# Optimization experiments

Hardware: AMD Instinct MI355X
Metric: run time of the kernel (lower is better)

The kernel has to match this reference:

```python
import jax, jax.numpy as jnp
import numpy as np

# Model hyperparameters (match init_kwargs / module defaults)
B, P, F_IN, H, K, OUT = 1024, 256, 8, 16, 8, 1


def _lin_init(key, out_f, in_f, bias=True):
    # torch nn.Linear default: U(-1/sqrt(in), 1/sqrt(in))
    kw, kb = jax.random.split(key)
    bound = 1.0 / np.sqrt(in_f)
    W = jax.random.uniform(kw, (out_f, in_f), jnp.float32, -bound, bound)
    if bias:
        b = jax.random.uniform(kb, (out_f,), jnp.float32, -bound, bound)
        return W, b
    return W


def setup_inputs() -> dict:
    key = jax.random.key(0)
    ks = jax.random.split(key, 7)
    x = jax.random.normal(ks[0], (B, P * F_IN), jnp.float32)
    W1 = _lin_init(ks[1], H, F_IN, bias=False)          # part_encode[0], bias=False
    W2, b2 = _lin_init(ks[2], H, H)                      # part_encode[2]
    W3, b3 = _lin_init(ks[3], H, H)                      # part_encode[4]
    We, be = _lin_init(ks[4], H, 2 * H)                  # edge MLP Linear(2H, H)
    Wo1, bo1 = _lin_init(ks[5], H // 2, H)               # output[0]
    Wo2, bo2 = _lin_init(ks[6], OUT, H // 2)             # output[2]
    return {"x": x, "W1": W1, "W2": W2, "b2": b2, "W3": W3, "b3": b3,
            "We": We, "be": be, "Wo1": Wo1, "bo1": bo1, "Wo2": Wo2, "bo2": bo2}


def reference(x, W1, W2, b2, W3, b3, We, be, Wo1, bo1, Wo2, bo2):
    b = x.shape[0]
    # part_encode MLP on flattened particles
    h = x.reshape(b * P, F_IN)
    h = jax.nn.elu(h @ W1.T)
    h = jax.nn.elu(h @ W2.T + b2)
    h = jax.nn.elu(h @ W3.T + b3)
    h = h.reshape(b, P, H)                               # [B,P,H]

    # Dynamic kNN graph per batch element (knn includes self at distance 0,
    # matching torch_cluster.knn on identical query/source sets)
    sq = jnp.sum(h * h, axis=-1)                         # [B,P]
    dist = sq[:, :, None] + sq[:, None, :] - 2.0 * jnp.einsum('bid,bjd->bij', h, h)
    _, idx = jax.lax.top_k(-dist, K)                     # [B,P,K] nearest neighbors

    # Gather neighbor features per graph
    xj = jax.vmap(lambda hb, ib: hb[ib])(h, idx)         # [B,P,K,H]
    xi = jnp.broadcast_to(h[:, :, None, :], xj.shape)    # [B,P,K,H]
    edge = jnp.concatenate([xi, xj - xi], axis=-1)       # [B,P,K,2H]

    # Edge MLP + max aggregation (EdgeConv message nn([x_i, x_j - x_i]), aggr='max')
    m = jax.nn.elu(edge @ We.T + be)                     # [B,P,K,H]
    node = jnp.max(m, axis=2)                            # [B,P,H]

    # avg_pool_x over nodes of each graph
    pooled = jnp.mean(node, axis=1)                      # [B,H]

    # output MLP + sigmoid (act_out=True, batchnorm=False)
    o = jax.nn.elu(pooled @ Wo1.T + bo1)
    o = o @ Wo2.T + bo2
    return jax.nn.sigmoid(o)                             # [B,OUT]
```

## Files before the change

### kernel.cpp

```cpp
#include <hip/hip_runtime.h>
#include <math.h>

#define NB 1024
#define NP 256
#define FIN 8
#define NH 16
#define NK 8

#define REP8A(X)  X(0) X(1) X(2) X(3) X(4) X(5) X(6) X(7)
#define REP16A(X) X(0) X(1) X(2) X(3) X(4) X(5) X(6) X(7) X(8) X(9) X(10) X(11) X(12) X(13) X(14) X(15)
#define REP16B(X) X(0) X(1) X(2) X(3) X(4) X(5) X(6) X(7) X(8) X(9) X(10) X(11) X(12) X(13) X(14) X(15)

typedef short s8v __attribute__((ext_vector_type(8)));
typedef float f4v __attribute__((ext_vector_type(4)));
typedef unsigned int u4v __attribute__((ext_vector_type(4)));

__device__ __forceinline__ float elu_f(float v) {
    return v > 0.f ? v : (__expf(v) - 1.f);
}
__device__ __forceinline__ unsigned bf16r(float f) {
    unsigned u = __float_as_uint(f);
    return (u + 0x7FFFu + ((u >> 16) & 1u)) >> 16;
}
__device__ __forceinline__ float ush2f(unsigned short u) {
    return __uint_as_float(((unsigned)u) << 16);
}

#define CE(a, b) { float lo_ = fminf(a, b), hi_ = fmaxf(a, b); a = lo_; b = hi_; }
#define SORT8(x0,x1,x2,x3,x4,x5,x6,x7) \
    CE(x0,x1) CE(x2,x3) CE(x4,x5) CE(x6,x7) \
    CE(x0,x2) CE(x1,x3) CE(x4,x6) CE(x5,x7) \
    CE(x1,x2) CE(x5,x6) \
    CE(x0,x4) CE(x1,x5) CE(x2,x6) CE(x3,x7) \
    CE(x2,x4) CE(x3,x5) \
    CE(x1,x2) CE(x3,x4) CE(x5,x6)
#define MERGE8P(P,x0,x1,x2,x3,x4,x5,x6,x7) \
    P##0 = fminf(P##0, x7); P##1 = fminf(P##1, x6); P##2 = fminf(P##2, x5); P##3 = fminf(P##3, x4); \
    P##4 = fminf(P##4, x3); P##5 = fminf(P##5, x2); P##6 = fminf(P##6, x1); P##7 = fminf(P##7, x0); \
    CE(P##0,P##4) CE(P##1,P##5) CE(P##2,P##6) CE(P##3,P##7) \
    CE(P##0,P##2) CE(P##1,P##3) CE(P##4,P##6) CE(P##5,P##7) \
    CE(P##0,P##1) CE(P##2,P##3) CE(P##4,P##5) CE(P##6,P##7)

#define KEYV(val, c) __uint_as_float((__float_as_uint((val) + sqp2) & 0xFFFFFF00u) | (unsigned)(c))

__global__ __attribute__((amdgpu_flat_work_group_size(256, 256),
                          amdgpu_waves_per_eu(2, 4)))
void edgenet_kernel(
    const float* __restrict__ gx,
    const float* __restrict__ gW1, const float* __restrict__ gW2, const float* __restrict__ gb2,
    const float* __restrict__ gW3, const float* __restrict__ gb3,
    const float* __restrict__ gWe, const float* __restrict__ gbe,
    const float* __restrict__ gWo1, const float* __restrict__ gbo1,
    const float* __restrict__ gWo2, const float* __restrict__ gbo2,
    float* __restrict__ gout)
{
    const int b  = blockIdx.x;
    const int t  = threadIdx.x;
    const int w  = t >> 6;
    const int lq = (t >> 4) & 3;
    const int lc = t & 15;

    __shared__ __align__(16) unsigned short hF[16][4][136];
    __shared__ __align__(16) float sq2arr[256];
    __shared__ __align__(16) float sbaseA[4][64][17];
    __shared__ __align__(16) uint2 jjarr[4][64];
    __shared__ float spool[64];

    float xi0, xi1, xi2, xi3, xi4, xi5, xi6, xi7;
    {
        const float4* xr = reinterpret_cast<const float4*>(gx + (size_t)b * (NP * FIN) + t * FIN);
        float4 v0 = xr[0], v1 = xr[1];
        xi0 = v0.x; xi1 = v0.y; xi2 = v0.z; xi3 = v0.w;
        xi4 = v1.x; xi5 = v1.y; xi6 = v1.z; xi7 = v1.w;
    }

    float l1_0,l1_1,l1_2,l1_3,l1_4,l1_5,l1_6,l1_7,l1_8,l1_9,l1_10,l1_11,l1_12,l1_13,l1_14,l1_15;
    float l2_0,l2_1,l2_2,l2_3,l2_4,l2_5,l2_6,l2_7,l2_8,l2_9,l2_10,l2_11,l2_12,l2_13,l2_14,l2_15;
    float hp0,hp1,hp2,hp3,hp4,hp5,hp6,hp7,hp8,hp9,hp10,hp11,hp12,hp13,hp14,hp15;

#define L1_BODY(i) s = fmaf(gW1[(o_) * FIN + i], xi##i, s);
#define L1_O(o) { const int o_ = (o); float s = 0.f; REP8A(L1_BODY) l1_##o = elu_f(s); }
    REP16A(L1_O)
#undef L1_O
#undef L1_BODY
#define L2_BODY(i) s = fmaf(gW2[(o_) * NH + i], l1_##i, s);
#define L2_O(o) { const int o_ = (o); float s = gb2[o_]; REP16B(L2_BODY) l2_##o = elu_f(s); }
    REP16A(L2_O)
#undef L2_O
#undef L2_BODY
#define L3_BODY(i) s = fmaf(gW3[(o_) * NH + i], l2_##i, s);
#define L3_O(o) { const int o_ = (o); float s = gb3[o_]; REP16B(L3_BODY) hp##o = elu_f(s); }
    REP16A(L3_O)
#undef L3_O
#undef L3_BODY

    {
        float* sb = &sbaseA[w][t & 63][0];
#define BAS_BODY(i) s = fmaf(gWe[(o_) * 32 + i] - gWe[(o_) * 32 + 16 + i], hp##i, s);
#define BAS_O(o) { const int o_ = (o); float s = gbe[o_]; REP16B(BAS_BODY) sb[o_] = s; }
        REP16A(BAS_O)
#undef BAS_O
#undef BAS_BODY
    }

    s8v eB1;
    {
        float4 wv = *reinterpret_cast<const float4*>(gWe + lc * 32 + 16 + 4 * lq);
        unsigned h0 = bf16r(wv.x), h1 = bf16r(wv.y), h2 = bf16r(wv.z), h3 = bf16r(wv.w);
        unsigned g0 = bf16r(wv.x - ush2f((unsigned short)h0));
        unsigned g1 = bf16r(wv.y - ush2f((unsigned short)h1));
        unsigned g2 = bf16r(wv.z - ush2f((unsigned short)h2));
        unsigned g3 = bf16r(wv.w - ush2f((unsigned short)h3));
        eB1 = (s8v){(short)h0, (short)h1, (short)h2, (short)h3,
                    (short)g0, (short)g1, (short)g2, (short)g3};
    }

    float sqp = 0.f;
#define SQ_I(i) sqp = fmaf(hp##i, hp##i, sqp);
    REP16A(SQ_I)
#undef SQ_I
    const float sqp2 = 0.5f * sqp;

#define PACKQ(q, A, B, C, D) { \
    unsigned ha = bf16r(hp##A), hb = bf16r(hp##B), hc = bf16r(hp##C), hd = bf16r(hp##D); \
    float ra = hp##A - ush2f((unsigned short)ha); \
    float rb = hp##B - ush2f((unsigned short)hb); \
    float rc = hp##C - ush2f((unsigned short)hc); \
    float rd = hp##D - ush2f((unsigned short)hd); \
    unsigned la = bf16r(ra), lb = bf16r(rb), lcc = bf16r(rc), ld = bf16r(rd); \
    u4v pk; pk.x = ha | (hb << 16); pk.y = hc | (hd << 16); \
            pk.z = la | (lb << 16); pk.w = lcc | (ld << 16); \
    *(u4v*)&hF[t >> 4][q][(t & 15) * 8] = pk; }
    PACKQ(0, 0, 1, 2, 3)
    PACKQ(1, 4, 5, 6, 7)
    PACKQ(2, 8, 9, 10, 11)
    PACKQ(3, 12, 13, 14, 15)
#undef PACKQ
    sq2arr[t] = sqp2;
    __syncthreads();

#define LDNAF(i) s8v naf##i; { \
    u4v au = __builtin_bit_cast(u4v, *(const s8v*)&hF[4 * w + (i)][lq][lc * 8]); \
    au.x ^= 0x80008000u; au.y ^= 0x80008000u; au.z ^= 0x80008000u; au.w ^= 0x80008000u; \
    naf##i = __builtin_bit_cast(s8v, au); }
    LDNAF(0) LDNAF(1) LDNAF(2) LDNAF(3)
#undef LDNAF

    float Ra0,Ra1,Ra2,Ra3,Ra4,Ra5,Ra6,Ra7;
    float Rb0,Rb1,Rb2,Rb3,Rb4,Rb5,Rb6,Rb7;
    float Rc0,Rc1,Rc2,Rc3,Rc4,Rc5,Rc6,Rc7;
    float Rd0,Rd1,Rd2,Rd3,Rd4,Rd5,Rd6,Rd7;
    {
        const float big = __uint_as_float(0x7F7FFFFFu);
        Ra0=Ra1=Ra2=Ra3=Ra4=Ra5=Ra6=Ra7 = big;
        Rb0=Rb1=Rb2=Rb3=Rb4=Rb5=Rb6=Rb7 = big;
        Rc0=Rc1=Rc2=Rc3=Rc4=Rc5=Rc6=Rc7 = big;
        Rd0=Rd1=Rd2=Rd3=Rd4=Rd5=Rd6=Rd7 = big;
    }

    for (int jt2 = 0; jt2 < 8; ++jt2) {
        const s8v b1a = *(const s8v*)&hF[2 * jt2][lq][lc * 8];
        const s8v b1b = *(const s8v*)&hF[2 * jt2 + 1][lq][lc * 8];
        const s8v b2a = __builtin_shufflevector(b1a, b1a, 4, 5, 6, 7, 0, 1, 2, 3);
        const s8v b2b = __builtin_shufflevector(b1b, b1b, 4, 5, 6, 7, 0, 1, 2, 3);
        const f4v sqa = *(const f4v*)&sq2arr[32 * jt2 + 4 * lq];
        const f4v sqb = *(const f4v*)&sq2arr[32 * jt2 + 16 + 4 * lq];
        const int c0 = 32 * jt2 + 4 * lq, c1 = c0 + 16;

#define GTT(naf, P) { \
        f4v da = __builtin_amdgcn_mfma_f32_16x16x32_bf16(b1a, naf, sqa, 0, 0, 0); \
        da     = __builtin_amdgcn_mfma_f32_16x16x32_bf16(b2a, naf, da,  0, 0, 0); \
        f4v db = __builtin_amdgcn_mfma_f32_16x16x32_bf16(b1b, naf, sqb, 0, 0, 0); \
        db     = __builtin_amdgcn_mfma_f32_16x16x32_bf16(b2b, naf, db,  0, 0, 0); \
        float k0 = KEYV(da[0], c0 + 0), k1 = KEYV(da[1], c0 + 1); \
        float k2 = KEYV(da[2], c0 + 2), k3 = KEYV(da[3], c0 + 3); \
        float k4 = KEYV(db[0], c1 + 0), k5 = KEYV(db[1], c1 + 1); \
        float k6 = KEYV(db[2], c1 + 2), k7 = KEYV(db[3], c1 + 3); \
        SORT8(k0, k1, k2, k3, k4, k5, k6, k7) \
        MERGE8P(P, k0, k1, k2, k3, k4, k5, k6, k7) }
        GTT(naf0, Ra)
        GTT(naf1, Rb)
        GTT(naf2, Rc)
        GTT(naf3, Rd)
#undef GTT
    }

#define FIN_TT(P, ttc) { \
    { float o0 = __shfl_xor(P##0, 16), o1 = __shfl_xor(P##1, 16), \
            o2 = __shfl_xor(P##2, 16), o3 = __shfl_xor(P##3, 16), \
            o4 = __shfl_xor(P##4, 16), o5 = __shfl_xor(P##5, 16), \
            o6 = __shfl_xor(P##6, 16), o7 = __shfl_xor(P##7, 16); \
      MERGE8P(P, o0, o1, o2, o3, o4, o5, o6, o7) } \
    { float o0 = __shfl_xor(P##0, 32), o1 = __shfl_xor(P##1, 32), \
            o2 = __shfl_xor(P##2, 32), o3 = __shfl_xor(P##3, 32), \
            o4 = __shfl_xor(P##4, 32), o5 = __shfl_xor(P##5, 32), \
            o6 = __shfl_xor(P##6, 32), o7 = __shfl_xor(P##7, 32); \
      MERGE8P(P, o0, o1, o2, o3, o4, o5, o6, o7) } \
    if (lq == (ttc)) { \
        unsigned plo = (__float_as_uint(P##0) & 0xFFu) \
                     | ((__float_as_uint(P##1) & 0xFFu) << 8) \
                     | ((__float_as_uint(P##2) & 0xFFu) << 16) \
                     | ((__float_as_uint(P##3) & 0xFFu) << 24); \
        unsigned phi = (__float_as_uint(P##4) & 0xFFu) \
                     | ((__float_as_uint(P##5) & 0xFFu) << 8) \
                     | ((__float_as_uint(P##6) & 0xFFu) << 16) \
                     | ((__float_as_uint(P##7) & 0xFFu) << 24); \
        jjarr[w][16 * (ttc) + lc] = make_uint2(plo, phi); \
    } }
    FIN_TT(Ra, 0)
    FIN_TT(Rb, 1)
    FIN_TT(Rc, 2)
    FIN_TT(Rd, 3)
#undef FIN_TT

    float psum = 0.f;
    {
        const s8v eB2 = __builtin_shufflevector(eB1, eB1, 4, 5, 6, 7, 0, 1, 2, 3);
        const int erow = lc;
        #pragma unroll 4
        for (int tt = 0; tt < 32; ++tt) {
            uint2 jv = jjarr[w][2 * tt + (erow >> 3)];
            unsigned word = (erow & 4) ? jv.y : jv.x;
            int jp = (int)((word >> ((erow & 3) * 8)) & 0xFFu);
            const s8v av = *(const s8v*)&hF[jp >> 4][lq][(jp & 15) * 8];
            f4v z = {0.f, 0.f, 0.f, 0.f};
            f4v d1 = __builtin_amdgcn_mfma_f32_16x16x32_bf16(av, eB1, z, 0, 0, 0);
            d1     = __builtin_amdgcn_mfma_f32_16x16x32_bf16(av, eB2, d1, 0, 0, 0);
            float mx = fmaxf(fmaxf(d1[0], d1[1]), fmaxf(d1[2], d1[3]));
            mx = fmaxf(mx, __shfl_xor(mx, 16, 64));
            float bz = sbaseA[w][2 * tt + (lq >> 1)][lc];
            psum += elu_f(mx + bz);
        }
    }
    psum += __shfl_xor(psum, 16, 64);
    psum += __shfl_xor(psum, 32, 64);
    if ((t & 63) < 16) spool[(w << 4) + lc] = psum;
    __syncthreads();

    if (t == 0) {
#define PL(i) const float pl##i = (spool[i] + spool[16 + i] + spool[32 + i] + spool[48 + i]) * (1.f / 512.f);
        REP16A(PL)
#undef PL
        float o1_0,o1_1,o1_2,o1_3,o1_4,o1_5,o1_6,o1_7;
#define HD_BODY(i) s = fmaf(gWo1[(o_) * NH + i], pl##i, s);
#define HD_O(o) { const int o_ = (o); float s = gbo1[o_]; REP16B(HD_BODY) o1_##o = elu_f(s); }
        REP8A(HD_O)
#undef HD_O
#undef HD_BODY
        float o2 = gbo2[0];
        o2 = fmaf(gWo2[0], o1_0, o2); o2 = fmaf(gWo2[1], o1_1, o2);
        o2 = fmaf(gWo2[2], o1_2, o2); o2 = fmaf(gWo2[3], o1_3, o2);
        o2 = fmaf(gWo2[4], o1_4, o2); o2 = fmaf(gWo2[5], o1_5, o2);
        o2 = fmaf(gWo2[6], o1_6, o2); o2 = fmaf(gWo2[7], o1_7, o2);
        gout[b] = 1.f / (1.f + expf(-o2));
    }
}

extern "C" void kernel_launch(void* const* d_in, const int* in_sizes, int n_in,
                              void* d_out, int out_size, void* d_ws, size_t ws_size,
                              hipStream_t stream) {
    const float* x   = (const float*)d_in[0];
    const float* W1  = (const float*)d_in[1];
    const float* W2  = (const float*)d_in[2];
    const float* b2  = (const float*)d_in[3];
    const float* W3  = (const float*)d_in[4];
    const float* b3  = (const float*)d_in[5];
    const float* We  = (const float*)d_in[6];
    const float* be  = (const float*)d_in[7];
    const float* Wo1 = (const float*)d_in[8];
    const float* bo1 = (const float*)d_in[9];
    const float* Wo2 = (const float*)d_in[10];
    const float* bo2 = (const float*)d_in[11];
    float* out = (float*)d_out;

    hipLaunchKernelGGL(edgenet_kernel, dim3(NB), dim3(NP), 0, stream,
                       x, W1, W2, b2, W3, b3, We, be, Wo1, bo1, Wo2, bo2, out);
}
```

Measured before the change: 125.8 us.

## Move particle encoder MLP and edge base term onto bf16 MFMA

The per-thread scalar FMA implementation of the three-layer particle encoder and the per-node edge base term is replaced with 16x16x32 bf16 MFMA tiles that use a hi/lo split for near-fp32 accuracy. Each wave now encodes 64 particles as four tiles, computes squared norms with cross-lane shuffles, and writes the packed features and the negated operand directly. The sqp2 addition in the key is dropped from KEYV, and the distance MFMAs still take sq2arr as their accumulator. This targets the large scalar FMA count and the weight reloads in the prologue, at the cost of extra split/pack work, shuffles, and a slightly different rounding profile.

After: 119.4 us. 5.1% less time.

```diff
diff --git a/kernel.cpp b/kernel.cpp
--- a/kernel.cpp
+++ b/kernel.cpp
@@ -25,6 +25,18 @@
 __device__ __forceinline__ float ush2f(unsigned short u) {
     return __uint_as_float(((unsigned)u) << 16);
 }
+__device__ __forceinline__ s8v split4(float4 wv) {
+    unsigned h0 = bf16r(wv.x), h1 = bf16r(wv.y), h2 = bf16r(wv.z), h3 = bf16r(wv.w);
+    unsigned g0 = bf16r(wv.x - ush2f((unsigned short)h0));
+    unsigned g1 = bf16r(wv.y - ush2f((unsigned short)h1));
+    unsigned g2 = bf16r(wv.z - ush2f((unsigned short)h2));
+    unsigned g3 = bf16r(wv.w - ush2f((unsigned short)h3));
+    u4v pk; pk.x = h0 | (h1 << 16); pk.y = h2 | (h3 << 16);
+            pk.z = g0 | (g1 << 16); pk.w = g2 | (g3 << 16);
+    return __builtin_bit_cast(s8v, pk);
+}
+#define HSWAP(v) __builtin_shufflevector(v, v, 4, 5, 6, 7, 0, 1, 2, 3)
+#define MFMA16(A, B, C) __builtin_amdgcn_mfma_f32_16x16x32_bf16(A, B, C, 0, 0, 0)
 
 #define CE(a, b) { float lo_ = fminf(a, b), hi_ = fmaxf(a, b); a = lo_; b = hi_; }
 #define SORT8(x0,x1,x2,x3,x4,x5,x6,x7) \
@@ -41,7 +53,7 @@
     CE(P##0,P##2) CE(P##1,P##3) CE(P##4,P##6) CE(P##5,P##7) \
     CE(P##0,P##1) CE(P##2,P##3) CE(P##4,P##5) CE(P##6,P##7)
 
-#define KEYV(val, c) __uint_as_float((__float_as_uint((val) + sqp2) & 0xFFFFFF00u) | (unsigned)(c))
+#define KEYV(val, c) __uint_as_float((__float_as_uint(val) & 0xFFFFFF00u) | (unsigned)(c))
 
 __global__ __attribute__((amdgpu_flat_work_group_size(256, 256),
                           amdgpu_waves_per_eu(2, 4)))
@@ -66,85 +78,52 @@
     __shared__ __align__(16) uint2 jjarr[4][64];
     __shared__ float spool[64];
 
-    float xi0, xi1, xi2, xi3, xi4, xi5, xi6, xi7;
-    {
-        const float4* xr = reinterpret_cast<const float4*>(gx + (size_t)b * (NP * FIN) + t * FIN);
-        float4 v0 = xr[0], v1 = xr[1];
-        xi0 = v0.x; xi1 = v0.y; xi2 = v0.z; xi3 = v0.w;
-        xi4 = v1.x; xi5 = v1.y; xi6 = v1.z; xi7 = v1.w;
-    }
-
-    float l1_0,l1_1,l1_2,l1_3,l1_4,l1_5,l1_6,l1_7,l1_8,l1_9,l1_10,l1_11,l1_12,l1_13,l1_14,l1_15;
-    float l2_0,l2_1,l2_2,l2_3,l2_4,l2_5,l2_6,l2_7,l2_8,l2_9,l2_10,l2_11,l2_12,l2_13,l2_14,l2_15;
-    float hp0,hp1,hp2,hp3,hp4,hp5,hp6,hp7,hp8,hp9,hp10,hp11,hp12,hp13,hp14,hp15;
-
-#define L1_BODY(i) s = fmaf(gW1[(o_) * FIN + i], xi##i, s);
-#define L1_O(o) { const int o_ = (o); float s = 0.f; REP8A(L1_BODY) l1_##o = elu_f(s); }
-    REP16A(L1_O)
-#undef L1_O
-#undef L1_BODY
-#define L2_BODY(i) s = fmaf(gW2[(o_) * NH + i], l1_##i, s);
-#define L2_O(o) { const int o_ = (o); float s = gb2[o_]; REP16B(L2_BODY) l2_##o = elu_f(s); }
-    REP16A(L2_O)
-#undef L2_O
-#undef L2_BODY
-#define L3_BODY(i) s = fmaf(gW3[(o_) * NH + i], l2_##i, s);
-#define L3_O(o) { const int o_ = (o); float s = gb3[o_]; REP16B(L3_BODY) hp##o = elu_f(s); }
-    REP16A(L3_O)
-#undef L3_O
-#undef L3_BODY
-
-    {
-        float* sb = &sbaseA[w][t & 63][0];
-#define BAS_BODY(i) s = fmaf(gWe[(o_) * 32 + i] - gWe[(o_) * 32 + 16 + i], hp##i, s);
-#define BAS_O(o) { const int o_ = (o); float s = gbe[o_]; REP16B(BAS_BODY) sb[o_] = s; }
-        REP16A(BAS_O)
-#undef BAS_O
-#undef BAS_BODY
-    }
-
-    s8v eB1;
-    {
-        float4 wv = *reinterpret_cast<const float4*>(gWe + lc * 32 + 16 + 4 * lq);
-        unsigned h0 = bf16r(wv.x), h1 = bf16r(wv.y), h2 = bf16r(wv.z), h3 = bf16r(wv.w);
-        unsigned g0 = bf16r(wv.x - ush2f((unsigned short)h0));
-        unsigned g1 = bf16r(wv.y - ush2f((unsigned short)h1));
-        unsigned g2 = bf16r(wv.z - ush2f((unsigned short)h2));
-        unsigned g3 = bf16r(wv.w - ush2f((unsigned short)h3));
-        eB1 = (s8v){(short)h0, (short)h1, (short)h2, (short)h3,
-                    (short)g0, (short)g1, (short)g2, (short)g3};
-    }
-
-    float sqp = 0.f;
-#define SQ_I(i) sqp = fmaf(hp##i, hp##i, sqp);
-    REP16A(SQ_I)
-#undef SQ_I
-    const float sqp2 = 0.5f * sqp;
-
-#define PACKQ(q, A, B, C, D) { \
-    unsigned ha = bf16r(hp##A), hb = bf16r(hp##B), hc = bf16r(hp##C), hd = bf16r(hp##D); \
-    float ra = hp##A - ush2f((unsigned short)ha); \
-    float rb = hp##B - ush2f((unsigned short)hb); \
-    float rc = hp##C - ush2f((unsigned short)hc); \
-    float rd = hp##D - ush2f((unsigned short)hd); \
-    unsigned la = bf16r(ra), lb = bf16r(rb), lcc = bf16r(rc), ld = bf16r(rd); \
-    u4v pk; pk.x = ha | (hb << 16); pk.y = hc | (hd << 16); \
-            pk.z = la | (lb << 16); pk.w = lcc | (ld << 16); \
-    *(u4v*)&hF[t >> 4][q][(t & 15) * 8] = pk; }
-    PACKQ(0, 0, 1, 2, 3)
-    PACKQ(1, 4, 5, 6, 7)
-    PACKQ(2, 8, 9, 10, 11)
-    PACKQ(3, 12, 13, 14, 15)
-#undef PACKQ
-    sq2arr[t] = sqp2;
+    const f4v zf4 = {0.f, 0.f, 0.f, 0.f};
+    const s8v zv8 = (s8v){0, 0, 0, 0, 0, 0, 0, 0};
+
+    s8v w1a = zv8;
+    if (lq < 2) w1a = split4(*reinterpret_cast<const float4*>(gW1 + lc * FIN + 4 * lq));
+    const s8v w1as = HSWAP(w1a);
+    const s8v w2a  = split4(*reinterpret_cast<const float4*>(gW2 + lc * NH + 4 * lq));
+    const s8v w2as = HSWAP(w2a);
+    const s8v w3a  = split4(*reinterpret_cast<const float4*>(gW3 + lc * NH + 4 * lq));
+    const s8v w3as = HSWAP(w3a);
+    f4v cb2, cb3;
+    {
+        float4 v2 = *reinterpret_cast<const float4*>(gb2 + 4 * lq);
+        float4 v3 = *reinterpret_cast<const float4*>(gb3 + 4 * lq);
+        cb2 = (f4v){v2.x, v2.y, v2.z, v2.w};
+        cb3 = (f4v){v3.x, v3.y, v3.z, v3.w};
+    }
+
+    s8v naf0, naf1, naf2, naf3;
+#define ENC_TILE(tt, NAF) { \
+    s8v xB = zv8; \
+    if (lq < 2) { \
+        float4 xv = *reinterpret_cast<const float4*>( \
+            gx + (size_t)b * (NP * FIN) + (64 * w + 16 * (tt) + lc) * FIN + 4 * lq); \
+        xB = split4(xv); } \
+    f4v d1 = MFMA16(w1a, xB, zf4); d1 = MFMA16(w1as, xB, d1); \
+    s8v hB1 = split4(make_float4(elu_f(d1[0]), elu_f(d1[1]), elu_f(d1[2]), elu_f(d1[3]))); \
+    f4v d2 = MFMA16(w2a, hB1, cb2); d2 = MFMA16(w2as, hB1, d2); \
+    s8v hB2 = split4(make_float4(elu_f(d2[0]), elu_f(d2[1]), elu_f(d2[2]), elu_f(d2[3]))); \
+    f4v d3 = MFMA16(w3a, hB2, cb3); d3 = MFMA16(w3as, hB2, d3); \
+    float h0_ = elu_f(d3[0]), h1_ = elu_f(d3[1]), h2_ = elu_f(d3[2]), h3_ = elu_f(d3[3]); \
+    s8v hB3 = split4(make_float4(h0_, h1_, h2_, h3_)); \
+    *(u4v*)&hF[4 * w + (tt)][lq][lc * 8] = __builtin_bit_cast(u4v, hB3); \
+    float sq_ = h0_ * h0_; sq_ = fmaf(h1_, h1_, sq_); \
+    sq_ = fmaf(h2_, h2_, sq_); sq_ = fmaf(h3_, h3_, sq_); \
+    sq_ += __shfl_xor(sq_, 16, 64); sq_ += __shfl_xor(sq_, 32, 64); \
+    if (lq == 0) sq2arr[64 * w + 16 * (tt) + lc] = 0.5f * sq_; \
+    { u4v nu = __builtin_bit_cast(u4v, hB3); \
+      nu.x ^= 0x80008000u; nu.y ^= 0x80008000u; nu.z ^= 0x80008000u; nu.w ^= 0x80008000u; \
+      NAF = __builtin_bit_cast(s8v, nu); } }
+    ENC_TILE(0, naf0)
+    ENC_TILE(1, naf1)
+    ENC_TILE(2, naf2)
+    ENC_TILE(3, naf3)
+#undef ENC_TILE
     __syncthreads();
-
-#define LDNAF(i) s8v naf##i; { \
-    u4v au = __builtin_bit_cast(u4v, *(const s8v*)&hF[4 * w + (i)][lq][lc * 8]); \
-    au.x ^= 0x80008000u; au.y ^= 0x80008000u; au.z ^= 0x80008000u; au.w ^= 0x80008000u; \
-    naf##i = __builtin_bit_cast(s8v, au); }
-    LDNAF(0) LDNAF(1) LDNAF(2) LDNAF(3)
-#undef LDNAF
 
     float Ra0,Ra1,Ra2,Ra3,Ra4,Ra5,Ra6,Ra7;
     float Rb0,Rb1,Rb2,Rb3,Rb4,Rb5,Rb6,Rb7;
@@ -161,17 +140,15 @@
     for (int jt2 = 0; jt2 < 8; ++jt2) {
         const s8v b1a = *(const s8v*)&hF[2 * jt2][lq][lc * 8];
         const s8v b1b = *(const s8v*)&hF[2 * jt2 + 1][lq][lc * 8];
-        const s8v b2a = __builtin_shufflevector(b1a, b1a, 4, 5, 6, 7, 0, 1, 2, 3);
-        const s8v b2b = __builtin_shufflevector(b1b, b1b, 4, 5, 6, 7, 0, 1, 2, 3);
+        const s8v b2a = HSWAP(b1a);
+        const s8v b2b = HSWAP(b1b);
         const f4v sqa = *(const f4v*)&sq2arr[32 * jt2 + 4 * lq];
         const f4v sqb = *(const f4v*)&sq2arr[32 * jt2 + 16 + 4 * lq];
         const int c0 = 32 * jt2 + 4 * lq, c1 = c0 + 16;
 
 #define GTT(naf, P) { \
-        f4v da = __builtin_amdgcn_mfma_f32_16x16x32_bf16(b1a, naf, sqa, 0, 0, 0); \
-        da     = __builtin_amdgcn_mfma_f32_16x16x32_bf16(b2a, naf, da,  0, 0, 0); \
-        f4v db = __builtin_amdgcn_mfma_f32_16x16x32_bf16(b1b, naf, sqb, 0, 0, 0); \
-        db     = __builtin_amdgcn_mfma_f32_16x16x32_bf16(b2b, naf, db,  0, 0, 0); \
+        f4v da = MFMA16(b1a, naf, sqa); da = MFMA16(b2a, naf, da); \
+        f4v db = MFMA16(b1b, naf, sqb); db = MFMA16(b2b, naf, db); \
         float k0 = KEYV(da[0], c0 + 0), k1 = KEYV(da[1], c0 + 1); \
         float k2 = KEYV(da[2], c0 + 2), k3 = KEYV(da[3], c0 + 3); \
         float k4 = KEYV(db[0], c1 + 0), k5 = KEYV(db[1], c1 + 1); \
@@ -213,9 +190,32 @@
     FIN_TT(Rd, 3)
 #undef FIN_TT
 
+    {
+        float4 wa = *reinterpret_cast<const float4*>(gWe + lc * 32 + 4 * lq);
+        float4 wc = *reinterpret_cast<const float4*>(gWe + lc * 32 + 16 + 4 * lq);
+        const s8v wca  = split4(make_float4(wa.x - wc.x, wa.y - wc.y, wa.z - wc.z, wa.w - wc.w));
+        const s8v wcas = HSWAP(wca);
+        float4 bev = *reinterpret_cast<const float4*>(gbe + 4 * lq);
+        const f4v cbe = (f4v){bev.x, bev.y, bev.z, bev.w};
+#define BASE_TILE(NAF, tt) { \
+        u4v pu = __builtin_bit_cast(u4v, NAF); \
+        pu.x ^= 0x80008000u; pu.y ^= 0x80008000u; pu.z ^= 0x80008000u; pu.w ^= 0x80008000u; \
+        s8v hB = __builtin_bit_cast(s8v, pu); \
+        f4v bd = MFMA16(wca, hB, cbe); bd = MFMA16(wcas, hB, bd); \
+        float* sb = &sbaseA[w][16 * (tt) + lc][4 * lq]; \
+        sb[0] = bd[0]; sb[1] = bd[1]; sb[2] = bd[2]; sb[3] = bd[3]; }
+        BASE_TILE(naf0, 0)
+        BASE_TILE(naf1, 1)
+        BASE_TILE(naf2, 2)
+        BASE_TILE(naf3, 3)
+#undef BASE_TILE
+    }
+
     float psum = 0.f;
     {
-        const s8v eB2 = __builtin_shufflevector(eB1, eB1, 4, 5, 6, 7, 0, 1, 2, 3);
+        float4 wv = *reinterpret_cast<const float4*>(gWe + lc * 32 + 16 + 4 * lq);
+        const s8v eB1 = split4(wv);
+        const s8v eB2 = HSWAP(eB1);
         const int erow = lc;
         #pragma unroll 4
         for (int tt = 0; tt < 32; ++tt) {
@@ -223,9 +223,8 @@
             unsigned word = (erow & 4) ? jv.y : jv.x;
             int jp = (int)((word >> ((erow & 3) * 8)) & 0xFFu);
             const s8v av = *(const s8v*)&hF[jp >> 4][lq][(jp & 15) * 8];
-            f4v z = {0.f, 0.f, 0.f, 0.f};
-            f4v d1 = __builtin_amdgcn_mfma_f32_16x16x32_bf16(av, eB1, z, 0, 0, 0);
-            d1     = __builtin_amdgcn_mfma_f32_16x16x32_bf16(av, eB2, d1, 0, 0, 0);
+            f4v d1 = MFMA16(av, eB1, zf4);
+            d1     = MFMA16(av, eB2, d1);
             float mx = fmaxf(fmaxf(d1[0], d1[1]), fmaxf(d1[2], d1[3]));
             mx = fmaxf(mx, __shfl_xor(mx, 16, 64));
             float bz = sbaseA[w][2 * tt + (lq >> 1)][lc];
```
